# Kernel optimization log

Hardware: AMD Instinct MI355X
Metric: run time of the kernel (lower is better)

## Reference

```python
import jax, jax.numpy as jnp
import numpy as np

B, S, D, H = 4096, 200, 64, 36
BN_EPS = 1e-5
DICE_EPS = 1e-3


def setup_inputs() -> dict:
    key = jax.random.key(0)
    ks = jax.random.split(key, 6)
    return {
        "history": jax.random.normal(ks[0], (B, S, D), dtype=jnp.float32),
        "candidate": jax.random.normal(ks[1], (B, D), dtype=jnp.float32),
        "W1": jax.random.normal(ks[2], (4 * D, H), dtype=jnp.float32) * 0.05,
        "b1": jax.random.normal(ks[3], (H,), dtype=jnp.float32) * 0.05,
        "gamma": jnp.ones((H,), dtype=jnp.float32),
        "beta": jnp.zeros((H,), dtype=jnp.float32),
        "alpha": jax.random.normal(ks[4], (1,), dtype=jnp.float32),
        "W2": jax.random.normal(ks[5], (H, 1), dtype=jnp.float32) * 0.05,
        "b2": jnp.zeros((1,), dtype=jnp.float32),
    }


def reference(history, candidate, W1, b1, gamma, beta, alpha, W2, b2):
    b, s, d = history.shape
    cand = jnp.broadcast_to(candidate[:, None, :], (b, s, d))
    att_in = jnp.concatenate([cand, history, cand - history, cand * history], axis=-1)
    x = att_in.reshape(b * s, 4 * d)
    # Linear
    h = x @ W1 + b1
    # BatchNorm1d (training mode: batch statistics, biased variance)
    mu = h.mean(axis=0)
    var = h.var(axis=0)
    h = (h - mu) * jax.lax.rsqrt(var + BN_EPS) * gamma + beta
    # Dice: per-row normalization over features, eps=1e-3
    avg = h.mean(axis=1, keepdims=True)
    v = jnp.sum((h - avg) ** 2, axis=1, keepdims=True) / h.shape[1]
    ps = jax.nn.sigmoid((h - avg) / jnp.sqrt(v + DICE_EPS))
    h = ps * h + (1.0 - ps) * alpha * h
    # Output linear -> attention weight per (b, s)
    w = (h @ W2 + b2).reshape(b, s)
    # Weighted sum pooling over sequence
    return jnp.einsum("bs,bsd->bd", w, history)
```

## Files before the change

### kernel.cpp

```cpp
#include <hip/hip_runtime.h>
#include <hip/hip_bf16.h>
#include <math.h>

#define BB 4096
#define SS 200
#define DD 64
#define HH 36
#define NP 48
#define NTI 13
#define NROWSF (4096.0f * 200.0f)
#define PSTRIDE 80
#define BPB 8
#define NBLK (BB / BPB)

typedef short bf16x8 __attribute__((ext_vector_type(8)));
typedef float f32x4 __attribute__((ext_vector_type(4)));

__device__ __forceinline__ unsigned short f2bf(float f) {
    union { float f; unsigned u; } v; v.f = f;
    unsigned r = v.u + 0x7FFFu + ((v.u >> 16) & 1u);
    return (unsigned short)(r >> 16);
}
__device__ __forceinline__ unsigned f2bf2(float a, float b) {
    union { __hip_bfloat162 h; unsigned u; } v;
    v.h = __float22bfloat162_rn(float2{a, b});
    return v.u;
}

__device__ __forceinline__ void gl_lds16(const void* g, void* l) {
    __builtin_amdgcn_global_load_lds(
        (const __attribute__((address_space(1))) unsigned*)g,
        (__attribute__((address_space(3))) unsigned*)l, 16, 0, 0);
}


__global__ __launch_bounds__(256) void k_wb(const float* __restrict__ cand,
                                            const float* __restrict__ W1,
                                            const float* __restrict__ b1,
                                            unsigned short* __restrict__ WbG,
                                            float* __restrict__ baseG) {
    int b = blockIdx.x, t = threadIdx.x;
    __shared__ float shC[DD];
    if (t < DD) shC[t] = cand[b * DD + t];
    __syncthreads();
    unsigned short* wb = WbG + (size_t)b * (NP * DD);
#pragma unroll
    for (int u = 0; u < 12; ++u) {
        int e = t + u * 256;
        int n = e >> 6, k = e & 63;
        float val = 0.f;
        if (n < HH)
            val = W1[(DD + k) * HH + n] - W1[(2 * DD + k) * HH + n] +
                  shC[k] * W1[(3 * DD + k) * HH + n];
        wb[e] = f2bf(val);
    }
    if (t < NP) {
        float v = 0.f;
        if (t < HH) {
            v = b1[t];
            for (int k = 0; k < DD; ++k)
                v += shC[k] * (W1[k * HH + t] + W1[(2 * DD + k) * HH + t]);
        }
        baseG[b * NP + t] = v;
    }
}

__device__ __forceinline__ void issue_loads(int b, int t,
                                            const float* __restrict__ hist,
                                            const unsigned short* __restrict__ WbG,
                                            const float* __restrict__ baseG,
                                            float4 (&v)[7], uint4& w, float& bse) {
    const float4* src = (const float4*)(hist + (size_t)b * SS * DD);
#pragma unroll
    for (int u = 0; u < 6; ++u) v[u] = src[t + u * 512];
    if (t < 128) v[6] = src[t + 3072];
    const uint4* wsrc = (const uint4*)(WbG + (size_t)b * (NP * DD));
    if (t < 384) w = wsrc[t];
    if (t < NP) bse = baseG[b * NP + t];
}

__device__ __forceinline__ void commit(int t, const float4 (&v)[7], const uint4& w,
                                       float bse, float* shHf,
                                       unsigned short* shWbT, float* shBase) {
#pragma unroll
    for (int u = 0; u < 6; ++u) {
        int G = t + u * 512;
        int sw = (G & ~15) | ((G & 15) ^ ((G >> 4) & 15));
        *(float4*)&shHf[sw * 4] = v[u];
    }
    if (t < 128) {
        int G = t + 3072;
        int sw = (G & ~15) | ((G & 15) ^ ((G >> 4) & 15));
        *(float4*)&shHf[sw * 4] = v[6];
    }
    if (t < 384) *(uint4*)((char*)shWbT + t * 16) = w;
    if (t < NP) shBase[t] = bse;
}

__device__ __forceinline__ void load_bfrags(const unsigned short* shWbT, int lane,
                                            bf16x8 (&bfr)[3][2]) {
    int col = lane & 15, q = lane >> 4;
#pragma unroll
    for (int nt = 0; nt < 3; ++nt)
#pragma unroll
        for (int kt = 0; kt < 2; ++kt)
            bfr[nt][kt] = *(const bf16x8*)&shWbT[(nt * 16 + col) * DD + kt * 32 + q * 8];
}

__device__ __forceinline__ bf16x8 load_afrag(const float* shHf, int m, int kt, int q) {
    int s0 = kt * 8 + q * 2;
    int x = m & 15;
    f32x4 x0 = *(const f32x4*)(shHf + m * DD + ((s0 ^ x) << 2));
    f32x4 x1 = *(const f32x4*)(shHf + m * DD + (((s0 + 1) ^ x) << 2));
    union { bf16x8 b8; unsigned u[4]; } a;
    a.u[0] = f2bf2(x0[0], x0[1]);
    a.u[1] = f2bf2(x0[2], x0[3]);
    a.u[2] = f2bf2(x1[0], x1[1]);
    a.u[3] = f2bf2(x1[2], x1[3]);
    return a.b8;
}

__device__ __forceinline__ void gemm_tile(const float* shHf,
                                          const bf16x8 (&bfr)[3][2], int mt, int lane,
                                          f32x4 (&d)[3]) {
    int m = mt * 16 + (lane & 15), q = lane >> 4;
    d[0] = f32x4{0.f, 0.f, 0.f, 0.f};
    d[1] = f32x4{0.f, 0.f, 0.f, 0.f};
    d[2] = f32x4{0.f, 0.f, 0.f, 0.f};
#pragma unroll
    for (int kt = 0; kt < 2; ++kt) {
        bf16x8 a = load_afrag(shHf, m, kt, q);
#pragma unroll
        for (int nt = 0; nt < 3; ++nt)
            d[nt] = __builtin_amdgcn_mfma_f32_16x16x32_bf16(a, bfr[nt][kt], d[nt], 0, 0, 0);
    }
}

__global__ __launch_bounds__(512, 4) void k_pass1m(const float* __restrict__ hist,
                                                   const unsigned short* __restrict__ WbG,
                                                   const float* __restrict__ baseG,
                                                   float* __restrict__ pstat) {
    __shared__ __align__(16) float shHf[(SS + 8) * DD];
    __shared__ __align__(16) unsigned short shWbT[NP * DD];
    __shared__ float shBase[NP];
    __shared__ float shP1[8][NP], shP2[8][NP];
    int t = threadIdx.x, wave = t >> 6, lane = t & 63;
    int col = lane & 15, q = lane >> 4;
    int b0 = blockIdx.x * BPB;

    if (t < 128)
        *(float4*)&shHf[SS * DD + t * 4] = float4{0.f, 0.f, 0.f, 0.f};
    {
        float4 v[7]; uint4 w; float bse = 0.f;
        issue_loads(b0, t, hist, WbG, baseG, v, w, bse);
        commit(t, v, w, bse, shHf, shWbT, shBase);
    }
    __syncthreads();

    for (int i = 0; i < BPB; ++i) {
        int b = b0 + i;
        float4 nv[7]; uint4 nw; float nbse = 0.f;
        if (i + 1 < BPB)
            issue_loads(b0 + i + 1, t, hist, WbG, baseG, nv, nw, nbse);

        bf16x8 bfr[3][2];
        load_bfrags(shWbT, lane, bfr);
        float basev[3];
#pragma unroll
        for (int nt = 0; nt < 3; ++nt) basev[nt] = shBase[nt * 16 + col];

        float cs1[3] = {0.f, 0.f, 0.f}, cs2[3] = {0.f, 0.f, 0.f};
        for (int mt = wave; mt < NTI; mt += 8) {
            f32x4 d[3];
            gemm_tile(shHf, bfr, mt, lane, d);
            if (mt == 12) {
                int grow0 = 192 + q * 4;
#pragma unroll
                for (int nt = 0; nt < 3; ++nt)
#pragma unroll
                    for (int r = 0; r < 4; ++r)
                        if (grow0 + r < SS) {
                            float vv = d[nt][r] + basev[nt];
                            cs1[nt] += vv;
                            cs2[nt] += vv * vv;
                        }
            } else {
#pragma unroll
                for (int nt = 0; nt < 3; ++nt)
#pragma unroll
                    for (int r = 0; r < 4; ++r) {
                        float vv = d[nt][r] + basev[nt];
                        cs1[nt] += vv;
                        cs2[nt] += vv * vv;
                    }
            }
        }
#pragma unroll
        for (int nt = 0; nt < 3; ++nt) {
            cs1[nt] += __shfl_xor(cs1[nt], 16);
            cs1[nt] += __shfl_xor(cs1[nt], 32);
            cs2[nt] += __shfl_xor(cs2[nt], 16);
            cs2[nt] += __shfl_xor(cs2[nt], 32);
        }
        if (lane < 16) {
#pragma unroll
            for (int nt = 0; nt < 3; ++nt) {
                shP1[wave][nt * 16 + lane] = cs1[nt];
                shP2[wave][nt * 16 + lane] = cs2[nt];
            }
        }
        __syncthreads();
        if (t < HH) {
            float s = 0.f;
#pragma unroll
            for (int w8 = 0; w8 < 8; ++w8) s += shP1[w8][t];
            pstat[(size_t)b * PSTRIDE + t] = s;
        } else if (t < 2 * HH) {
            int f = t - HH;
            float s = 0.f;
#pragma unroll
            for (int w8 = 0; w8 < 8; ++w8) s += shP2[w8][f];
            pstat[(size_t)b * PSTRIDE + t] = s;
        }
        if (i + 1 < BPB) {
            commit(t, nv, nw, nbse, shHf, shWbT, shBase);
            __syncthreads();
        }
    }
}

__global__ __launch_bounds__(512, 4) void k_pass2m(const float* __restrict__ hist,
                                                   const unsigned short* __restrict__ WbG,
                                                   const float* __restrict__ baseG,
                                                   const float* __restrict__ Acoef,
                                                   const float* __restrict__ Bcoef,
                                                   const float* __restrict__ alpha,
                                                   const float* __restrict__ W2,
                                                   const float* __restrict__ b2,
                                                   float* __restrict__ out) {
    __shared__ __align__(16) float shHf[(SS + 8) * DD];
    __shared__ __align__(16) unsigned short shWbT[NP * DD];
    __shared__ float shBase[NP];
    __shared__ float shW[(SS + 8)];
    __shared__ float shPool[8][DD];
    int t = threadIdx.x, wave = t >> 6, lane = t & 63;
    int col = lane & 15, q = lane >> 4;
    int b0 = blockIdx.x * BPB;

    float Ar[3], Bcr[3], W2r[3];
#pragma unroll
    for (int nt = 0; nt < 3; ++nt) {
        int c = nt * 16 + col;
        Ar[nt] = Acoef[c];
        Bcr[nt] = Bcoef[c];
        W2r[nt] = (c < HH) ? W2[c] : 0.f;
    }
    float alv = alpha[0], one_m_alv = 1.0f - alv, b2v = b2[0];

    if (t < 128)
        *(float4*)&shHf[SS * DD + t * 4] = float4{0.f, 0.f, 0.f, 0.f};
    {
        float4 v[7]; uint4 w; float bse = 0.f;
        issue_loads(b0, t, hist, WbG, baseG, v, w, bse);
        commit(t, v, w, bse, shHf, shWbT, shBase);
    }
    __syncthreads();

    for (int i = 0; i < BPB; ++i) {
        int b = b0 + i;
        float4 nv[7]; uint4 nw; float nbse = 0.f;
        if (i + 1 < BPB)
            issue_loads(b0 + i + 1, t, hist, WbG, baseG, nv, nw, nbse);

        bf16x8 bfr[3][2];
        load_bfrags(shWbT, lane, bfr);
        float baseAB[3];
#pragma unroll
        for (int nt = 0; nt < 3; ++nt)
            baseAB[nt] = fmaf(shBase[nt * 16 + col], Ar[nt], Bcr[nt]);

        for (int mt = wave; mt < NTI; mt += 8) {
            f32x4 d[3];
            gemm_tile(shHf, bfr, mt, lane, d);
            float hp[3][4];
#pragma unroll
            for (int nt = 0; nt < 3; ++nt)
#pragma unroll
                for (int r = 0; r < 4; ++r)
                    hp[nt][r] = fmaf(d[nt][r], Ar[nt], baseAB[nt]);
            float s1[4], s2[4], wsum[4];
#pragma unroll
            for (int r = 0; r < 4; ++r) {
                s1[r] = hp[0][r] + hp[1][r] + hp[2][r];
                s2[r] = hp[0][r] * hp[0][r] + hp[1][r] * hp[1][r] + hp[2][r] * hp[2][r];
                s1[r] += __shfl_xor(s1[r], 1);
                s1[r] += __shfl_xor(s1[r], 2);
                s1[r] += __shfl_xor(s1[r], 4);
                s1[r] += __shfl_xor(s1[r], 8);
                s2[r] += __shfl_xor(s2[r], 1);
                s2[r] += __shfl_xor(s2[r], 2);
                s2[r] += __shfl_xor(s2[r], 4);
                s2[r] += __shfl_xor(s2[r], 8);
            }
#pragma unroll
            for (int r = 0; r < 4; ++r) {
                float avg = s1[r] * (1.0f / (float)HH);
                float var = s2[r] * (1.0f / (float)HH) - avg * avg;
                float inv = rsqrtf(var + 1e-3f);
                float wv = 0.f;
#pragma unroll
                for (int nt = 0; nt < 3; ++nt) {
                    float z = (hp[nt][r] - avg) * inv;
                    float ps = 1.0f / (1.0f + __expf(-z));
                    float f = fmaf(ps, one_m_alv, alv);
                    wv = fmaf(hp[nt][r] * f, W2r[nt], wv);
                }
                wsum[r] = wv;
                wsum[r] += __shfl_xor(wsum[r], 1);
                wsum[r] += __shfl_xor(wsum[r], 2);
                wsum[r] += __shfl_xor(wsum[r], 4);
                wsum[r] += __shfl_xor(wsum[r], 8);
            }
            if (col == 0) {
                float4 o = {wsum[0] + b2v, wsum[1] + b2v, wsum[2] + b2v, wsum[3] + b2v};
                *(float4*)&shW[mt * 16 + q * 4] = o;
            }
        }
        __syncthreads();
        {
            float p = 0.f;
            for (int s = wave; s < SS; s += 8) {
                int sw = (((lane >> 2) ^ (s & 15)) << 2) | (lane & 3);
                p = fmaf(shW[s], shHf[s * DD + sw], p);
            }
            shPool[wave][lane] = p;
        }
        __syncthreads();
        if (t < DD) {
            float s = 0.f;
#pragma unroll
            for (int w8 = 0; w8 < 8; ++w8) s += shPool[w8][t];
            out[b * DD + t] = s;
        }
        if (i + 1 < BPB) {
            commit(t, nv, nw, nbse, shHf, shWbT, shBase);
            __syncthreads();
        }
    }
}

__global__ __launch_bounds__(256) void k_stats_red(const float* __restrict__ pstat,
                                                   const float* __restrict__ gamma,
                                                   const float* __restrict__ beta,
                                                   float* __restrict__ A,
                                                   float* __restrict__ Bc) {
    int f = blockIdx.x, t = threadIdx.x;
    if (f >= HH) {
        if (t == 0) { A[f] = 0.f; Bc[f] = 0.f; }
        return;
    }
    float s1 = 0.f, s2 = 0.f;
    for (int r = t; r < BB; r += 256) {
        s1 += pstat[(size_t)r * PSTRIDE + f];
        s2 += pstat[(size_t)r * PSTRIDE + HH + f];
    }
#pragma unroll
    for (int off = 1; off < 64; off <<= 1) {
        s1 += __shfl_xor(s1, off);
        s2 += __shfl_xor(s2, off);
    }
    __shared__ float a1[4], a2[4];
    if ((t & 63) == 0) { a1[t >> 6] = s1; a2[t >> 6] = s2; }
    __syncthreads();
    if (t == 0) {
        s1 = a1[0] + a1[1] + a1[2] + a1[3];
        s2 = a2[0] + a2[1] + a2[2] + a2[3];
        float mu = s1 * (1.0f / NROWSF);
        float var = s2 * (1.0f / NROWSF) - mu * mu;
        float a = rsqrtf(var + 1e-5f) * gamma[f];
        A[f] = a;
        Bc[f] = beta[f] - mu * a;
    }
}

__global__ void k_stats(const float* __restrict__ gsum, const float* __restrict__ gsum2,
                        const float* __restrict__ gamma, const float* __restrict__ beta,
                        float* __restrict__ A, float* __restrict__ Bc) {
    int t = threadIdx.x;
    if (t < NP) {
        if (t < HH) {
            float mu = gsum[t] * (1.0f / NROWSF);
            float var = gsum2[t] * (1.0f / NROWSF) - mu * mu;
            float a = rsqrtf(var + 1e-5f) * gamma[t];
            A[t] = a;
            Bc[t] = beta[t] - mu * a;
        } else {
            A[t] = 0.f;
            Bc[t] = 0.f;
        }
    }
}

__device__ __forceinline__ void prologue_fb(int b, int t,
                                            const float* __restrict__ hist,
                                            const float* __restrict__ cand,
                                            const float* __restrict__ W1,
                                            const float* __restrict__ b1,
                                            float* shHf, unsigned short* shWbT,
                                            float* shC, float* shBase,
                                            float (*shBaseP)[NP]) {
    if (t < DD) shC[t] = cand[b * DD + t];
    const float4* src = (const float4*)(hist + (size_t)b * SS * DD);
    float4 v[7];
#pragma unroll
    for (int u = 0; u < 6; ++u) v[u] = src[t + u * 512];
    if (t < 128) v[6] = src[t + 3072];
    if (t < 128)
        *(float4*)&shHf[SS * DD + t * 4] = float4{0.f, 0.f, 0.f, 0.f};
    __syncthreads();
#pragma unroll
    for (int u = 0; u < 6; ++u) {
        int G = t + u * 512;
        int sw = (G & ~15) | ((G & 15) ^ ((G >> 4) & 15));
        *(float4*)&shHf[sw * 4] = v[u];
    }
    if (t < 128) {
        int G = t + 3072;
        int sw = (G & ~15) | ((G & 15) ^ ((G >> 4) & 15));
        *(float4*)&shHf[sw * 4] = v[6];
    }
    for (int e = t; e < NP * DD; e += 512) {
        int n = e >> 6, k = e & 63;
        float val = 0.f;
        if (n < HH)
            val = W1[(DD + k) * HH + n] - W1[(2 * DD + k) * HH + n] +
                  shC[k] * W1[(3 * DD + k) * HH + n];
        shWbT[n * DD + k] = f2bf(val);
    }
    if (t < 4 * NP) {
        int g = t / NP, j = t - g * NP;
        float p = 0.f;
        if (j < HH) {
#pragma unroll 4
            for (int k = 16 * g; k < 16 * g + 16; ++k)
                p += shC[k] * (W1[k * HH + j] + W1[(2 * DD + k) * HH + j]);
        }
        shBaseP[g][j] = p;
    }
    __syncthreads();
    if (t < NP) {
        float val = (t < HH) ? b1[t] : 0.f;
        shBase[t] = val + shBaseP[0][t] + shBaseP[1][t] + shBaseP[2][t] +
                    shBaseP[3][t];
    }
    __syncthreads();
}

template <bool RED>
__global__ __launch_bounds__(512, 4) void k_pass1f(const float* __restrict__ hist,
                                                   const float* __restrict__ cand,
                                                   const float* __restrict__ W1,
                                                   const float* __restrict__ b1,
                                                   float* __restrict__ pstat,
                                                   float* __restrict__ gsum,
                                                   float* __restrict__ gsum2) {
    __shared__ __align__(16) float shHf[(SS + 8) * DD];
    __shared__ __align__(16) unsigned short shWbT[NP * DD];
    __shared__ float shC[DD], shBase[NP];
    __shared__ float shBaseP[4][NP];
    __shared__ float shP1[8][NP], shP2[8][NP];
    int b = blockIdx.x;
    int t = threadIdx.x, wave = t >> 6, lane = t & 63;
    int col = lane & 15, q = lane >> 4;

    prologue_fb(b, t, hist, cand, W1, b1, shHf, shWbT, shC, shBase, shBaseP);

    bf16x8 bfr[3][2];
    load_bfrags(shWbT, lane, bfr);
    float basev[3];
#pragma unroll
    for (int nt = 0; nt < 3; ++nt) basev[nt] = shBase[nt * 16 + col];

    float cs1[3] = {0.f, 0.f, 0.f}, cs2[3] = {0.f, 0.f, 0.f};
    for (int mt = wave; mt < NTI; mt += 8) {
        f32x4 d[3];
        gemm_tile(shHf, bfr, mt, lane, d);
        if (mt == 12) {
            int grow0 = 192 + q * 4;
#pragma unroll
            for (int nt = 0; nt < 3; ++nt)
#pragma unroll
                for (int r = 0; r < 4; ++r)
                    if (grow0 + r < SS) {
                        float vv = d[nt][r] + basev[nt];
                        cs1[nt] += vv;
                        cs2[nt] += vv * vv;
                    }
        } else {
#pragma unroll
            for (int nt = 0; nt < 3; ++nt)
#pragma unroll
                for (int r = 0; r < 4; ++r) {
                    float vv = d[nt][r] + basev[nt];
                    cs1[nt] += vv;
                    cs2[nt] += vv * vv;
                }
        }
    }
#pragma unroll
    for (int nt = 0; nt < 3; ++nt) {
        cs1[nt] += __shfl_xor(cs1[nt], 16);
        cs1[nt] += __shfl_xor(cs1[nt], 32);
        cs2[nt] += __shfl_xor(cs2[nt], 16);
        cs2[nt] += __shfl_xor(cs2[nt], 32);
    }
    if (lane < 16) {
#pragma unroll
        for (int nt = 0; nt < 3; ++nt) {
            shP1[wave][nt * 16 + lane] = cs1[nt];
            shP2[wave][nt * 16 + lane] = cs2[nt];
        }
    }
    __syncthreads();
    if (RED) {
        if (t < HH) {
            float s = 0.f;
#pragma unroll
            for (int w = 0; w < 8; ++w) s += shP1[w][t];
            pstat[(size_t)b * PSTRIDE + t] = s;
        } else if (t < 2 * HH) {
            int f = t - HH;
            float s = 0.f;
#pragma unroll
            for (int w = 0; w < 8; ++w) s += shP2[w][f];
            pstat[(size_t)b * PSTRIDE + t] = s;
        }
    } else {
        if (t < HH) {
            float s1 = 0.f, s2 = 0.f;
#pragma unroll
            for (int w = 0; w < 8; ++w) { s1 += shP1[w][t]; s2 += shP2[w][t]; }
            atomicAdd(gsum + t, s1);
            atomicAdd(gsum2 + t, s2);
        }
    }
}

__global__ __launch_bounds__(512, 4) void k_pass2f(const float* __restrict__ hist,
                                                   const float* __restrict__ cand,
                                                   const float* __restrict__ W1,
                                                   const float* __restrict__ b1,
                                                   const float* __restrict__ Acoef,
                                                   const float* __restrict__ Bcoef,
                                                   const float* __restrict__ alpha,
                                                   const float* __restrict__ W2,
                                                   const float* __restrict__ b2,
                                                   float* __restrict__ out) {
    __shared__ __align__(16) float shHf[(SS + 8) * DD];
    __shared__ __align__(16) unsigned short shWbT[NP * DD];
    __shared__ float shC[DD], shBase[NP];
    __shared__ float shBaseP[4][NP];
    __shared__ float shW[(SS + 8)];
    __shared__ float shPool[8][DD];
    int b = blockIdx.x;
    int t = threadIdx.x, wave = t >> 6, lane = t & 63;
    int col = lane & 15, q = lane >> 4;

    prologue_fb(b, t, hist, cand, W1, b1, shHf, shWbT, shC, shBase, shBaseP);

    bf16x8 bfr[3][2];
    load_bfrags(shWbT, lane, bfr);
    float baseAB[3], Ar[3], W2r[3];
#pragma unroll
    for (int nt = 0; nt < 3; ++nt) {
        int c = nt * 16 + col;
        Ar[nt] = Acoef[c];
        baseAB[nt] = fmaf(shBase[c], Ar[nt], Bcoef[c]);
        W2r[nt] = (c < HH) ? W2[c] : 0.f;
    }
    float alv = alpha[0], one_m_alv = 1.0f - alv, b2v = b2[0];

    for (int mt = wave; mt < NTI; mt += 8) {
        f32x4 d[3];
        gemm_tile(shHf, bfr, mt, lane, d);
        float hp[3][4];
#pragma unroll
        for (int nt = 0; nt < 3; ++nt)
#pragma unroll
            for (int r = 0; r < 4; ++r)
                hp[nt][r] = fmaf(d[nt][r], Ar[nt], baseAB[nt]);
        float s1[4], s2[4], wsum[4];
#pragma unroll
        for (int r = 0; r < 4; ++r) {
            s1[r] = hp[0][r] + hp[1][r] + hp[2][r];
            s2[r] = hp[0][r] * hp[0][r] + hp[1][r] * hp[1][r] + hp[2][r] * hp[2][r];
            s1[r] += __shfl_xor(s1[r], 1);
            s1[r] += __shfl_xor(s1[r], 2);
            s1[r] += __shfl_xor(s1[r], 4);
            s1[r] += __shfl_xor(s1[r], 8);
            s2[r] += __shfl_xor(s2[r], 1);
            s2[r] += __shfl_xor(s2[r], 2);
            s2[r] += __shfl_xor(s2[r], 4);
            s2[r] += __shfl_xor(s2[r], 8);
        }
#pragma unroll
        for (int r = 0; r < 4; ++r) {
            float avg = s1[r] * (1.0f / (float)HH);
            float var = s2[r] * (1.0f / (float)HH) - avg * avg;
            float inv = rsqrtf(var + 1e-3f);
            float wv = 0.f;
#pragma unroll
            for (int nt = 0; nt < 3; ++nt) {
                float z = (hp[nt][r] - avg) * inv;
                float ps = 1.0f / (1.0f + __expf(-z));
                float f = fmaf(ps, one_m_alv, alv);
                wv = fmaf(hp[nt][r] * f, W2r[nt], wv);
            }
            wsum[r] = wv;
            wsum[r] += __shfl_xor(wsum[r], 1);
            wsum[r] += __shfl_xor(wsum[r], 2);
            wsum[r] += __shfl_xor(wsum[r], 4);
            wsum[r] += __shfl_xor(wsum[r], 8);
        }
        if (col == 0) {
            float4 o = {wsum[0] + b2v, wsum[1] + b2v, wsum[2] + b2v, wsum[3] + b2v};
            *(float4*)&shW[mt * 16 + q * 4] = o;
        }
    }
    __syncthreads();
    {
        float p = 0.f;
        for (int s = wave; s < SS; s += 8) {
            int sw = (((lane >> 2) ^ (s & 15)) << 2) | (lane & 3);
            p = fmaf(shW[s], shHf[s * DD + sw], p);
        }
        shPool[wave][lane] = p;
    }
    __syncthreads();
    if (t < DD) {
        float s = 0.f;
#pragma unroll
        for (int w = 0; w < 8; ++w) s += shPool[w][t];
        out[b * DD + t] = s;
    }
}

extern "C" void kernel_launch(void* const* d_in, const int* in_sizes, int n_in,
                              void* d_out, int out_size, void* d_ws, size_t ws_size,
                              hipStream_t stream) {
    const float* hist = (const float*)d_in[0];
    const float* cand = (const float*)d_in[1];
    const float* W1 = (const float*)d_in[2];
    const float* b1 = (const float*)d_in[3];
    const float* gamma = (const float*)d_in[4];
    const float* beta = (const float*)d_in[5];
    const float* alpha = (const float*)d_in[6];
    const float* W2 = (const float*)d_in[7];
    const float* b2 = (const float*)d_in[8];
    float* out = (float*)d_out;
    float* ws = (float*)d_ws;

    const size_t pstatF = (size_t)BB * PSTRIDE;
    const size_t baseF = (size_t)BB * NP;
    const size_t wbBytes = (size_t)BB * NP * DD * 2;
    const size_t fullNeed = (pstatF + 2 * NP + baseF) * 4 + wbBytes;
    const size_t midNeed = (pstatF + 2 * NP) * 4;

    if (ws_size >= fullNeed) {
        float* pstat = ws;
        float* A = pstat + pstatF;
        float* Bc = A + NP;
        float* baseG = Bc + NP;
        unsigned short* WbG = (unsigned short*)(baseG + baseF);
        k_wb<<<BB, 256, 0, stream>>>(cand, W1, b1, WbG, baseG);
        k_pass1m<<<NBLK, 512, 0, stream>>>(hist, WbG, baseG, pstat);
        k_stats_red<<<NP, 256, 0, stream>>>(pstat, gamma, beta, A, Bc);
        k_pass2m<<<NBLK, 512, 0, stream>>>(hist, WbG, baseG, A, Bc, alpha, W2, b2,
                                           out);
    } else if (ws_size >= midNeed) {
        float* pstat = ws;
        float* A = pstat + pstatF;
        float* Bc = A + NP;
        k_pass1f<true><<<BB, 512, 0, stream>>>(hist, cand, W1, b1, pstat, nullptr,
                                               nullptr);
        k_stats_red<<<NP, 256, 0, stream>>>(pstat, gamma, beta, A, Bc);
        k_pass2f<<<BB, 512, 0, stream>>>(hist, cand, W1, b1, A, Bc, alpha, W2, b2,
                                         out);
    } else {
        float* gsum = ws;
        float* gsum2 = ws + NP;
        float* A = ws + 2 * NP;
        float* Bc = ws + 3 * NP;
        hipMemsetAsync(gsum, 0, 2 * NP * sizeof(float), stream);
        k_pass1f<false><<<BB, 512, 0, stream>>>(hist, cand, W1, b1, nullptr, gsum,
                                                gsum2);
        k_stats<<<1, 64, 0, stream>>>(gsum, gsum2, gamma, beta, A, Bc);
        k_pass2f<<<BB, 512, 0, stream>>>(hist, cand, W1, b1, A, Bc, alpha, W2, b2,
                                         out);
    }
}
```

Before: 513.1 us.

## Double-buffer LDS with async global-to-LDS loads in both passes

Both pass kernels no longer stage the next batch element through registers before copying it into shared memory. They now issue direct global-to-LDS loads into a second shared buffer, so the fetch for the next element overlaps the MFMA work on the current one. The XOR swizzle moves to the global source address. Batch elements per block go from 8 to 16 and launch bounds drop to 2 blocks per SM. This leaves one 512-thread block per CU with a larger LDS footprint, trading occupancy and inter-block latency hiding for in-block prefetch.

After: 458.6 us. 1.12x faster.

```diff
diff --git a/kernel.cpp b/kernel.cpp
--- a/kernel.cpp
+++ b/kernel.cpp
@@ -10,7 +10,7 @@
 #define NTI 13
 #define NROWSF (4096.0f * 200.0f)
 #define PSTRIDE 80
-#define BPB 8
+#define BPB 16
 #define NBLK (BB / BPB)
 
 typedef short bf16x8 __attribute__((ext_vector_type(8)));
@@ -65,36 +65,29 @@
     }
 }
 
-__device__ __forceinline__ void issue_loads(int b, int t,
-                                            const float* __restrict__ hist,
-                                            const unsigned short* __restrict__ WbG,
-                                            const float* __restrict__ baseG,
-                                            float4 (&v)[7], uint4& w, float& bse) {
-    const float4* src = (const float4*)(hist + (size_t)b * SS * DD);
-#pragma unroll
-    for (int u = 0; u < 6; ++u) v[u] = src[t + u * 512];
-    if (t < 128) v[6] = src[t + 3072];
-    const uint4* wsrc = (const uint4*)(WbG + (size_t)b * (NP * DD));
-    if (t < 384) w = wsrc[t];
-    if (t < NP) bse = baseG[b * NP + t];
-}
-
-__device__ __forceinline__ void commit(int t, const float4 (&v)[7], const uint4& w,
-                                       float bse, float* shHf,
-                                       unsigned short* shWbT, float* shBase) {
-#pragma unroll
-    for (int u = 0; u < 6; ++u) {
-        int G = t + u * 512;
-        int sw = (G & ~15) | ((G & 15) ^ ((G >> 4) & 15));
-        *(float4*)&shHf[sw * 4] = v[u];
+__device__ __forceinline__ void dma_b(int b, int t,
+                                      const float* __restrict__ hist,
+                                      const unsigned short* __restrict__ WbG,
+                                      const float* __restrict__ baseG,
+                                      float* dH, unsigned short* dW, float* dB) {
+    const char* hb = (const char*)(hist + (size_t)b * SS * DD);
+    char* lb = (char*)dH;
+#pragma unroll
+    for (int j = 0; j < 6; ++j) {
+        int idx = j * 512 + t;
+        int m = idx >> 4, sl = idx & 15;
+        gl_lds16(hb + (m << 8) + ((sl ^ (m & 15)) << 4), lb + idx * 16);
     }
     if (t < 128) {
-        int G = t + 3072;
-        int sw = (G & ~15) | ((G & 15) ^ ((G >> 4) & 15));
-        *(float4*)&shHf[sw * 4] = v[6];
-    }
-    if (t < 384) *(uint4*)((char*)shWbT + t * 16) = w;
-    if (t < NP) shBase[t] = bse;
+        int idx = 3072 + t;
+        int m = idx >> 4, sl = idx & 15;
+        gl_lds16(hb + (m << 8) + ((sl ^ (m & 15)) << 4), lb + idx * 16);
+    }
+    if (t < 384)
+        gl_lds16((const char*)(WbG + (size_t)b * (NP * DD)) + t * 16,
+                 (char*)dW + t * 16);
+    if (t >= 384 && t < 384 + NP)
+        dB[t - 384] = baseG[(size_t)b * NP + (t - 384)];
 }
 
 __device__ __forceinline__ void load_bfrags(const unsigned short* shWbT, int lane,
@@ -136,43 +129,47 @@
     }
 }
 
-__global__ __launch_bounds__(512, 4) void k_pass1m(const float* __restrict__ hist,
+__global__ __launch_bounds__(512, 2) void k_pass1p(const float* __restrict__ hist,
                                                    const unsigned short* __restrict__ WbG,
                                                    const float* __restrict__ baseG,
                                                    float* __restrict__ pstat) {
-    __shared__ __align__(16) float shHf[(SS + 8) * DD];
-    __shared__ __align__(16) unsigned short shWbT[NP * DD];
-    __shared__ float shBase[NP];
+    __shared__ __align__(16) float shHfA[(SS + 8) * DD];
+    __shared__ __align__(16) float shHfB[(SS + 8) * DD];
+    __shared__ __align__(16) unsigned short shWbA[NP * DD];
+    __shared__ __align__(16) unsigned short shWbB[NP * DD];
+    __shared__ float shBaseA[NP], shBaseB[NP];
     __shared__ float shP1[8][NP], shP2[8][NP];
     int t = threadIdx.x, wave = t >> 6, lane = t & 63;
     int col = lane & 15, q = lane >> 4;
     int b0 = blockIdx.x * BPB;
 
     if (t < 128)
-        *(float4*)&shHf[SS * DD + t * 4] = float4{0.f, 0.f, 0.f, 0.f};
-    {
-        float4 v[7]; uint4 w; float bse = 0.f;
-        issue_loads(b0, t, hist, WbG, baseG, v, w, bse);
-        commit(t, v, w, bse, shHf, shWbT, shBase);
-    }
+        *(float4*)&shHfA[SS * DD + t * 4] = float4{0.f, 0.f, 0.f, 0.f};
+    else if (t < 256)
+        *(float4*)&shHfB[SS * DD + (t - 128) * 4] = float4{0.f, 0.f, 0.f, 0.f};
+    dma_b(b0, t, hist, WbG, baseG, shHfA, shWbA, shBaseA);
     __syncthreads();
 
     for (int i = 0; i < BPB; ++i) {
         int b = b0 + i;
-        float4 nv[7]; uint4 nw; float nbse = 0.f;
+        const float* curH = (i & 1) ? shHfB : shHfA;
+        const unsigned short* curW = (i & 1) ? shWbB : shWbA;
+        const float* curB = (i & 1) ? shBaseB : shBaseA;
         if (i + 1 < BPB)
-            issue_loads(b0 + i + 1, t, hist, WbG, baseG, nv, nw, nbse);
+            dma_b(b + 1, t, hist, WbG, baseG,
+                  (i & 1) ? shHfA : shHfB, (i & 1) ? shWbA : shWbB,
+                  (i & 1) ? shBaseA : shBaseB);
 
         bf16x8 bfr[3][2];
-        load_bfrags(shWbT, lane, bfr);
+        load_bfrags(curW, lane, bfr);
         float basev[3];
 #pragma unroll
-        for (int nt = 0; nt < 3; ++nt) basev[nt] = shBase[nt * 16 + col];
+        for (int nt = 0; nt < 3; ++nt) basev[nt] = curB[nt * 16 + col];
 
         float cs1[3] = {0.f, 0.f, 0.f}, cs2[3] = {0.f, 0.f, 0.f};
         for (int mt = wave; mt < NTI; mt += 8) {
             f32x4 d[3];
-            gemm_tile(shHf, bfr, mt, lane, d);
+            gemm_tile(curH, bfr, mt, lane, d);
             if (mt == 12) {
                 int grow0 = 192 + q * 4;
 #pragma unroll
@@ -222,14 +219,11 @@
             for (int w8 = 0; w8 < 8; ++w8) s += shP2[w8][f];
             pstat[(size_t)b * PSTRIDE + t] = s;
         }
-        if (i + 1 < BPB) {
-            commit(t, nv, nw, nbse, shHf, shWbT, shBase);
-            __syncthreads();
-        }
-    }
-}
-
-__global__ __launch_bounds__(512, 4) void k_pass2m(const float* __restrict__ hist,
+        if (i + 1 < BPB) __syncthreads();
+    }
+}
+
+__global__ __launch_bounds__(512, 2) void k_pass2p(const float* __restrict__ hist,
                                                    const unsigned short* __restrict__ WbG,
                                                    const float* __restrict__ baseG,
                                                    const float* __restrict__ Acoef,
@@ -238,9 +232,11 @@
                                                    const float* __restrict__ W2,
                                                    const float* __restrict__ b2,
                                                    float* __restrict__ out) {
-    __shared__ __align__(16) float shHf[(SS + 8) * DD];
-    __shared__ __align__(16) unsigned short shWbT[NP * DD];
-    __shared__ float shBase[NP];
+    __shared__ __align__(16) float shHfA[(SS + 8) * DD];
+    __shared__ __align__(16) float shHfB[(SS + 8) * DD];
+    __shared__ __align__(16) unsigned short shWbA[NP * DD];
+    __shared__ __align__(16) unsigned short shWbB[NP * DD];
+    __shared__ float shBaseA[NP], shBaseB[NP];
     __shared__ float shW[(SS + 8)];
     __shared__ float shPool[8][DD];
     int t = threadIdx.x, wave = t >> 6, lane = t & 63;
@@ -258,30 +254,32 @@
     float alv = alpha[0], one_m_alv = 1.0f - alv, b2v = b2[0];
 
     if (t < 128)
-        *(float4*)&shHf[SS * DD + t * 4] = float4{0.f, 0.f, 0.f, 0.f};
-    {
-        float4 v[7]; uint4 w; float bse = 0.f;
-        issue_loads(b0, t, hist, WbG, baseG, v, w, bse);
-        commit(t, v, w, bse, shHf, shWbT, shBase);
-    }
+        *(float4*)&shHfA[SS * DD + t * 4] = float4{0.f, 0.f, 0.f, 0.f};
+    else if (t < 256)
+        *(float4*)&shHfB[SS * DD + (t - 128) * 4] = float4{0.f, 0.f, 0.f, 0.f};
+    dma_b(b0, t, hist, WbG, baseG, shHfA, shWbA, shBaseA);
     __syncthreads();
 
     for (int i = 0; i < BPB; ++i) {
         int b = b0 + i;
-        float4 nv[7]; uint4 nw; float nbse = 0.f;
+        const float* curH = (i & 1) ? shHfB : shHfA;
+        const unsigned short* curW = (i & 1) ? shWbB : shWbA;
+        const float* curB = (i & 1) ? shBaseB : shBaseA;
         if (i + 1 < BPB)
-            issue_loads(b0 + i + 1, t, hist, WbG, baseG, nv, nw, nbse);
+            dma_b(b + 1, t, hist, WbG, baseG,
+                  (i & 1) ? shHfA : shHfB, (i & 1) ? shWbA : shWbB,
+                  (i & 1) ? shBaseA : shBaseB);
 
         bf16x8 bfr[3][2];
-        load_bfrags(shWbT, lane, bfr);
+        load_bfrags(curW, lane, bfr);
         float baseAB[3];
 #pragma unroll
         for (int nt = 0; nt < 3; ++nt)
-            baseAB[nt] = fmaf(shBase[nt * 16 + col], Ar[nt], Bcr[nt]);
+            baseAB[nt] = fmaf(curB[nt * 16 + col], Ar[nt], Bcr[nt]);
 
         for (int mt = wave; mt < NTI; mt += 8) {
             f32x4 d[3];
-            gemm_tile(shHf, bfr, mt, lane, d);
+            gemm_tile(curH, bfr, mt, lane, d);
             float hp[3][4];
 #pragma unroll
             for (int nt = 0; nt < 3; ++nt)
@@ -331,7 +329,7 @@
             float p = 0.f;
             for (int s = wave; s < SS; s += 8) {
                 int sw = (((lane >> 2) ^ (s & 15)) << 2) | (lane & 3);
-                p = fmaf(shW[s], shHf[s * DD + sw], p);
+                p = fmaf(shW[s], curH[s * DD + sw], p);
             }
             shPool[wave][lane] = p;
         }
@@ -342,10 +340,7 @@
             for (int w8 = 0; w8 < 8; ++w8) s += shPool[w8][t];
             out[b * DD + t] = s;
         }
-        if (i + 1 < BPB) {
-            commit(t, nv, nw, nbse, shHf, shWbT, shBase);
-            __syncthreads();
-        }
+        if (i + 1 < BPB) __syncthreads();
     }
 }
 
@@ -673,9 +668,9 @@
         float* baseG = Bc + NP;
         unsigned short* WbG = (unsigned short*)(baseG + baseF);
         k_wb<<<BB, 256, 0, stream>>>(cand, W1, b1, WbG, baseG);
-        k_pass1m<<<NBLK, 512, 0, stream>>>(hist, WbG, baseG, pstat);
+        k_pass1p<<<NBLK, 512, 0, stream>>>(hist, WbG, baseG, pstat);
         k_stats_red<<<NP, 256, 0, stream>>>(pstat, gamma, beta, A, Bc);
-        k_pass2m<<<NBLK, 512, 0, stream>>>(hist, WbG, baseG, A, Bc, alpha, W2, b2,
+        k_pass2p<<<NBLK, 512, 0, stream>>>(hist, WbG, baseG, A, Bc, alpha, W2, b2,
                                            out);
     } else if (ws_size >= midNeed) {
         float* pstat = ws;
```
